# Kernel optimization log

Hardware: AMD Instinct MI355X
Metric: run time of the kernel (lower is better)

Reference implementation:

```python
import jax, jax.numpy as jnp
import numpy as np

EPS_ATTN = 1e-8  # self.eps is undefined in the torch source; standard slot-attention value
LN_EPS = 1e-5


def _ln(x, g=None, b=None, axes=(-1,)):
    m = x.mean(axes, keepdims=True)
    v = ((x - m) ** 2).mean(axes, keepdims=True)
    y = (x - m) * jax.lax.rsqrt(v + LN_EPS)
    return y * g + b if g is not None else y


def setup_inputs() -> dict:
    key = jax.random.key(0)
    ks = jax.random.split(key, 16)
    B, N, S, d, dh = 16, 4096, 8, 64, 128

    def w(k, shape, fan_in):
        return jax.random.normal(k, shape, jnp.float32) / np.float32(np.sqrt(fan_in))

    return {
        "inputs": jax.random.normal(ks[0], (B, N, d + 2), jnp.float32),
        "slots": jax.random.normal(ks[1], (S, d + 4), jnp.float32),
        "Wq": w(ks[2], (d, d), d),
        "Wk": w(ks[3], (d, d), d),
        "Wv": w(ks[4], (d, d), d),
        "Wg": w(ks[5], (d, 2), 2),
        "bg": jnp.zeros((d,), jnp.float32),
        "ln_pos_g": jnp.ones((d,), jnp.float32),
        "ln_pos_b": jnp.zeros((d,), jnp.float32),
        "W1": w(ks[6], (dh, d), d),
        "b1": jnp.zeros((dh,), jnp.float32),
        "W2": w(ks[7], (d, dh), dh),
        "b2": jnp.zeros((d,), jnp.float32),
        "W_ih": w(ks[8], (3 * d, d), d),
        "W_hh": w(ks[9], (3 * d, d), d),
        "b_ih": jnp.zeros((3 * d,), jnp.float32),
        "b_hh": jnp.zeros((3 * d,), jnp.float32),
        "ln_mlp_g": jnp.ones((d,), jnp.float32),
        "ln_mlp_b": jnp.zeros((d,), jnp.float32),
        "W3": w(ks[10], (dh, d), d),
        "b3": jnp.zeros((dh,), jnp.float32),
        "W4": w(ks[11], (d, dh), dh),
        "b4": jnp.zeros((d,), jnp.float32),
        "ln_slot_g": jnp.ones((d,), jnp.float32),
        "ln_slot_b": jnp.zeros((d,), jnp.float32),
        "n_iters": 3,
    }


def reference(inputs, slots, Wq, Wk, Wv, Wg, bg, ln_pos_g, ln_pos_b, W1, b1, W2, b2,
              W_ih, W_hh, b_ih, b_hh, ln_mlp_g, ln_mlp_b, W3, b3, W4, b4,
              ln_slot_g, ln_slot_b, n_iters):
    feats, grids = inputs[..., :-2], inputs[..., -2:]          # (B,N,d), (B,N,2)
    sl, pos, sc = slots[..., :-4], slots[..., -4:-2], slots[..., -2:]
    B, N, _ = feats.shape
    S, d = sl.shape
    scale = d ** (-0.5)

    slots = jnp.broadcast_to(sl, (B, S, d))
    positions = jnp.clip(jnp.broadcast_to(pos, (B, S, 2)), -1.0, 1.0)
    scales = jnp.clip(jnp.broadcast_to(sc, (B, S, 2)), 1e-3, 2.0)

    k = feats @ Wk.T                                           # (B,N,d)
    v = feats @ Wv.T

    def pos_mlp(x):  # LayerNorm -> Linear -> ReLU -> Linear
        h = _ln(x, ln_pos_g, ln_pos_b)
        h = jax.nn.relu(h @ W1.T + b1)
        return h @ W2.T + b2

    for i_iter in range(n_iters + 1):
        rel = (grids[:, :, None] - positions[:, None]) / scales[:, None]  # (B,N,S,2)
        rgp = rel @ Wg.T + bg                                             # (B,N,S,d)
        k_pos = pos_mlp(k[:, :, None] + rgp)                              # (B,N,S,d)
        v_pos = pos_mlp(v[:, :, None] + rgp)

        slots_n = _ln(slots, ln_slot_g, ln_slot_b)
        q = _ln(slots_n, axes=(-2, -1)) @ Wq.T                            # (B,S,d)

        dots = jnp.einsum('bsd,bnsd->bns', q, k_pos) * scale              # (B,N,S)
        attn = jax.nn.softmax(dots, axis=1) + EPS_ATTN
        attn = attn / attn.sum(axis=-1, keepdims=True)

        updates = jnp.einsum('bns,bnsd->bsd', attn, v_pos)                # (B,S,d)
        positions = jnp.einsum('bns,bnp->bsp', attn, grids)               # (B,S,2)
        spread = (grids[:, :, None] - positions[:, None]) ** 2            # (B,N,S,2)
        scales = jnp.clip(jnp.sqrt(jnp.einsum('bns,bnsp->bsp', attn, spread)), 1e-3, 2.0)

        if i_iter < n_iters:
            x = updates.reshape(-1, d)
            h = slots.reshape(-1, d)
            gi = x @ W_ih.T + b_ih
            gh = h @ W_hh.T + b_hh
            i_r, i_z, i_n = jnp.split(gi, 3, axis=-1)
            h_r, h_z, h_n = jnp.split(gh, 3, axis=-1)
            r = jax.nn.sigmoid(i_r + h_r)
            z = jax.nn.sigmoid(i_z + h_z)
            n_g = jnp.tanh(i_n + r * h_n)
            slots = ((1.0 - z) * n_g + z * h).reshape(B, S, d)
            # slot_mlp (no residual in the source)
            hmlp = jax.nn.relu(_ln(slots, ln_mlp_g, ln_mlp_b) @ W3.T + b3)
            slots = hmlp @ W4.T + b4

    return jnp.concatenate([slots, positions, scales], axis=-1)           # (B,S,d+4)
```

## Files before the change

### kernel.cpp

```cpp
#include <hip/hip_runtime.h>
#include <math.h>

#define BB 16
#define NN 4096
#define SS 8
#define DD 64
#define DHH 128
#define CIN 66
#define NITERS 3
#define LN_EPS_F 1e-5f
#define EPS_ATTN_F 1e-8f
#define QSCALE 0.125f
#define LO_SCALE 2048.0f
#define LO_INV 4.8828125e-4f

typedef __attribute__((ext_vector_type(8))) _Float16 half8;
typedef __attribute__((ext_vector_type(4))) float f32x4;
union H8 { half8 v; _Float16 u[8]; };

__device__ __forceinline__ float dot4(float4 a, float4 b) {
    return fmaf(a.x, b.x, fmaf(a.y, b.y, fmaf(a.z, b.z, a.w * b.w)));
}

__device__ __forceinline__ void split_fp16(float z, _Float16& h, _Float16& l) {
    _Float16 hh = (_Float16)z;
    float rem = (z - (float)hh) * LO_SCALE;
    h = hh;
    l = (_Float16)rem;
}

__global__ __launch_bounds__(256) void k_init_slots(
    const float* __restrict__ slots_in, float* __restrict__ slots,
    float* __restrict__ positions, float* __restrict__ scales) {
    int tid = blockIdx.x * 256 + threadIdx.x;
    if (tid < BB * SS * DD) {
        int s = (tid / DD) % SS;
        int c = tid % DD;
        slots[tid] = slots_in[s * 68 + c];
    }
    if (tid < BB * SS * 2) {
        int s = (tid >> 1) & 7;
        int p = tid & 1;
        float po = slots_in[s * 68 + 64 + p];
        positions[tid] = fminf(fmaxf(po, -1.f), 1.f);
        float sc = slots_in[s * 68 + 66 + p];
        scales[tid] = fminf(fmaxf(sc, 1e-3f), 2.f);
    }
}

__global__ __launch_bounds__(256) void k_prep_w(
    const float* __restrict__ W1, const float* __restrict__ lpg,
    const float* __restrict__ lpb, const float* __restrict__ b1,
    const float* __restrict__ Wg,
    float* __restrict__ W1p, float* __restrict__ avec, float* __restrict__ bvec,
    float* __restrict__ s1vec, float* __restrict__ b1p, float* __restrict__ wgc) {
    __shared__ float w1s[128 * 68];
    int tid = threadIdx.x;
    for (int q = 0; q < 8; q++) {
        int flat = q * 1024 + tid * 4;
        int o = flat >> 6, c = flat & 63;
        *(float4*)(w1s + o * 68 + c) = *(const float4*)(W1 + flat);
    }
    __syncthreads();
    if (tid < 128) {
        int o = tid;
        float a = 0.f, bv = 0.f, s1 = 0.f, b1a = b1[o];
        for (int c = 0; c < 64; c++) {
            float w0 = w1s[o * 68 + c];
            float w = w0 * lpg[c];
            W1p[o * 64 + c] = w;
            a = fmaf(w, Wg[2 * c], a);
            bv = fmaf(w, Wg[2 * c + 1], bv);
            s1 += w;
            b1a = fmaf(w0, lpb[c], b1a);
        }
        avec[o] = a; bvec[o] = bv; s1vec[o] = s1; b1p[o] = b1a;
    }
    if (tid == 128) {
        float mwA = 0.f, mwB = 0.f, AA = 0.f, BBv = 0.f, AB = 0.f;
        for (int c = 0; c < 64; c++) {
            float wa = Wg[2 * c], wb = Wg[2 * c + 1];
            mwA += wa; mwB += wb;
            AA = fmaf(wa, wa, AA); BBv = fmaf(wb, wb, BBv); AB = fmaf(wa, wb, AB);
        }
        wgc[0] = mwA * (1.f / 64.f);
        wgc[1] = mwB * (1.f / 64.f);
        wgc[2] = AA * (1.f / 64.f);
        wgc[3] = BBv * (1.f / 64.f);
        wgc[4] = AB * (2.f / 64.f);
    }
}

__global__ __launch_bounds__(256) void k_prep_w2(
    const float* __restrict__ W1p, const float* __restrict__ Wk,
    const float* __restrict__ Wv, const float* __restrict__ bg,
    float* __restrict__ Wall, float* __restrict__ cu) {
    int flat = blockIdx.x * 256 + threadIdx.x;
    int mat = flat >> 13, rem = flat & 8191;
    int o = rem >> 6, c = rem & 63;
    const float* Wm = mat ? Wv : Wk;
    float acc = 0.f;
    for (int d = 0; d < 64; d++)
        acc = fmaf(W1p[o * 64 + d], Wm[d * 64 + c], acc);
    Wall[flat] = acc;
    if (flat < 128) {
        float a = 0.f;
        for (int d = 0; d < 64; d++) a = fmaf(W1p[flat * 64 + d], bg[d], a);
        cu[flat] = a;
    }
}

__global__ __launch_bounds__(256) void k_prep_frag(
    const float* __restrict__ Wall, const float* __restrict__ Wk,
    const float* __restrict__ Wv,
    _Float16* __restrict__ cwh, _Float16* __restrict__ cwl,
    _Float16* __restrict__ mwh, _Float16* __restrict__ mwl) {
    int idx = blockIdx.x * 256 + threadIdx.x;
    if (idx < 2048) {
        int f = idx >> 6, lane = idx & 63;
        int m = f >> 4, rest = f & 15;
        int ot = rest >> 1, ks = rest & 1;
        int o = ot * 16 + (lane & 15);
        int k0 = ks * 32 + (lane >> 4) * 8;
        const float* src = Wall + m * 8192 + o * 64 + k0;
        #pragma unroll
        for (int j = 0; j < 8; j++) {
            _Float16 h, l;
            split_fp16(src[j], h, l);
            cwh[(size_t)f * 512 + lane * 8 + j] = h;
            cwl[(size_t)f * 512 + lane * 8 + j] = l;
        }
    } else if (idx < 3072) {
        int id2 = idx - 2048;
        int f = id2 >> 6, lane = id2 & 63;
        int m = f >> 3, rest = f & 7;
        int ot = rest >> 1, ks = rest & 1;
        int o = ot * 16 + (lane & 15);
        int k0 = ks * 32 + (lane >> 4) * 8;
        const float* src = (m ? Wv : Wk) + o * 64 + k0;
        #pragma unroll
        for (int j = 0; j < 8; j++) {
            _Float16 h, l;
            split_fp16(src[j], h, l);
            mwh[(size_t)f * 512 + lane * 8 + j] = h;
            mwl[(size_t)f * 512 + lane * 8 + j] = l;
        }
    }
}

__global__ __launch_bounds__(256) void k_prep_mfma(
    const float* __restrict__ inp,
    const _Float16* __restrict__ cwh, const _Float16* __restrict__ cwl,
    const _Float16* __restrict__ mwh, const _Float16* __restrict__ mwl,
    const float* __restrict__ cu, const float* __restrict__ bg,
    const float* __restrict__ Wg,
    float* __restrict__ uk, float* __restrict__ uv,
    float* __restrict__ kaux, float* __restrict__ vaux, float* __restrict__ gbuf) {
    __shared__ float T[4][16 * 132];
    int tid = threadIdx.x;
    int wv = tid >> 6, lane = tid & 63;
    int quad = lane >> 4, col = lane & 15;
    int mat = blockIdx.y;
    int rowTile = blockIdx.x * 64 + wv * 16;
    half8 ah[2], al[2];
    {
        int rA = rowTile + col;
        const float* rp = inp + (size_t)rA * CIN + quad * 8;
        #pragma unroll
        for (int ks = 0; ks < 2; ks++) {
            H8 h, l;
            #pragma unroll
            for (int q = 0; q < 4; q++) {
                float2 v = *(const float2*)(rp + ks * 32 + 2 * q);
                split_fp16(v.x, h.u[2 * q], l.u[2 * q]);
                split_fp16(v.y, h.u[2 * q + 1], l.u[2 * q + 1]);
            }
            ah[ks] = h.v; al[ks] = l.v;
        }
    }
    const _Float16* cwhm = cwh + (size_t)mat * 16 * 512;
    const _Float16* cwlm = cwl + (size_t)mat * 16 * 512;
    #pragma unroll
    for (int ot = 0; ot < 8; ot++) {
        f32x4 acc1 = {0.f, 0.f, 0.f, 0.f}, acc2 = {0.f, 0.f, 0.f, 0.f};
        #pragma unroll
        for (int ks = 0; ks < 2; ks++) {
            half8 bh = *(const half8*)(cwhm + (size_t)(ot * 2 + ks) * 512 + lane * 8);
            half8 bl = *(const half8*)(cwlm + (size_t)(ot * 2 + ks) * 512 + lane * 8);
            acc1 = __builtin_amdgcn_mfma_f32_16x16x32_f16(ah[ks], bh, acc1, 0, 0, 0);
            acc2 = __builtin_amdgcn_mfma_f32_16x16x32_f16(al[ks], bh, acc2, 0, 0, 0);
            acc2 = __builtin_amdgcn_mfma_f32_16x16x32_f16(ah[ks], bl, acc2, 0, 0, 0);
        }
        float cuv = cu[ot * 16 + col];
        #pragma unroll
        for (int r = 0; r < 4; r++) {
            float u = fmaf(acc2[r], LO_INV, acc1[r]) + cuv;
            T[wv][(quad * 4 + r) * 132 + ot * 16 + col] = u;
        }
    }
    const _Float16* mwhm = mwh + (size_t)mat * 8 * 512;
    const _Float16* mwlm = mwl + (size_t)mat * 8 * 512;
    float mk[4] = {0.f, 0.f, 0.f, 0.f}, kk2[4] = {0.f, 0.f, 0.f, 0.f};
    float kA[4] = {0.f, 0.f, 0.f, 0.f}, kB[4] = {0.f, 0.f, 0.f, 0.f};
    #pragma unroll
    for (int ot = 0; ot < 4; ot++) {
        f32x4 acc1 = {0.f, 0.f, 0.f, 0.f}, acc2 = {0.f, 0.f, 0.f, 0.f};
        #pragma unroll
        for (int ks = 0; ks < 2; ks++) {
            half8 bh = *(const half8*)(mwhm + (size_t)(ot * 2 + ks) * 512 + lane * 8);
            half8 bl = *(const half8*)(mwlm + (size_t)(ot * 2 + ks) * 512 + lane * 8);
            acc1 = __builtin_amdgcn_mfma_f32_16x16x32_f16(ah[ks], bh, acc1, 0, 0, 0);
            acc2 = __builtin_amdgcn_mfma_f32_16x16x32_f16(al[ks], bh, acc2, 0, 0, 0);
            acc2 = __builtin_amdgcn_mfma_f32_16x16x32_f16(ah[ks], bl, acc2, 0, 0, 0);
        }
        int o = ot * 16 + col;
        float bgo = bg[o], wa = Wg[2 * o], wb = Wg[2 * o + 1];
        #pragma unroll
        for (int r = 0; r < 4; r++) {
            float x = fmaf(acc2[r], LO_INV, acc1[r]) + bgo;
            mk[r] += x; kk2[r] = fmaf(x, x, kk2[r]);
            kA[r] = fmaf(x, wa, kA[r]); kB[r] = fmaf(x, wb, kB[r]);
        }
    }
    #pragma unroll
    for (int off = 1; off <= 8; off <<= 1) {
        #pragma unroll
        for (int r = 0; r < 4; r++) {
            mk[r] += __shfl_xor(mk[r], off, 64);
            kk2[r] += __shfl_xor(kk2[r], off, 64);
            kA[r] += __shfl_xor(kA[r], off, 64);
            kB[r] += __shfl_xor(kB[r], off, 64);
        }
    }
    float* aux = mat ? vaux : kaux;
    if (col == 0) {
        #pragma unroll
        for (int r = 0; r < 4; r++) {
            int row = rowTile + quad * 4 + r;
            float2 g = *(const float2*)(inp + (size_t)row * CIN + 64);
            float4 m1 = {mk[r] * (1.f / 64.f), kk2[r] * (1.f / 64.f),
                         kA[r] * (1.f / 32.f), kB[r] * (1.f / 32.f)};
            float4 m2 = {g.x, g.y, 0.f, 0.f};
            *(float4*)(aux + (size_t)row * 8) = m1;
            *(float4*)(aux + (size_t)row * 8 + 4) = m2;
            if (mat == 0) {
                float2 gw = {g.x, g.y};
                *(float2*)(gbuf + (size_t)row * 2) = gw;
            }
        }
    }
    __syncthreads();
    {
        float* dst = mat ? uv : uk;
        int r = lane >> 2, cseg = (lane & 3) * 32;
        const float* Tr = &T[wv][r * 132 + cseg];
        float* gp = dst + (size_t)(rowTile + r) * 128 + cseg;
        #pragma unroll
        for (int q = 0; q < 8; q++)
            *(float4*)(gp + 4 * q) = *(const float4*)(Tr + 4 * q);
    }
}

__global__ __launch_bounds__(512) void k_slot_prep(
    const float* __restrict__ slots, const float* __restrict__ lsg,
    const float* __restrict__ lsb, const float* __restrict__ Wq,
    const float* __restrict__ W2, const float* __restrict__ b2,
    float* __restrict__ w2q, float* __restrict__ qb2) {
    __shared__ float sn[512];
    __shared__ float qv[SS][64];
    __shared__ float wsum[8], wsum2[8];
    int b = blockIdx.x, t = threadIdx.x;
    int s = t >> 6, c = t & 63;
    float x = slots[(b * SS + s) * DD + c];
    float sum = x;
    for (int off = 32; off; off >>= 1) sum += __shfl_xor(sum, off, 64);
    float m = sum * (1.f / 64.f);
    float dv = x - m;
    float vs = dv * dv;
    for (int off = 32; off; off >>= 1) vs += __shfl_xor(vs, off, 64);
    float y = dv * rsqrtf(vs * (1.f / 64.f) + LN_EPS_F) * lsg[c] + lsb[c];
    float s1 = y, s2 = y * y;
    for (int off = 32; off; off >>= 1) { s1 += __shfl_xor(s1, off, 64); s2 += __shfl_xor(s2, off, 64); }
    if (c == 0) { wsum[s] = s1; wsum2[s] = s2; }
    __syncthreads();
    float ts1 = 0.f, ts2 = 0.f;
    #pragma unroll
    for (int i = 0; i < 8; i++) { ts1 += wsum[i]; ts2 += wsum2[i]; }
    float gm = ts1 * (1.f / 512.f);
    float gv = ts2 * (1.f / 512.f) - gm * gm;
    sn[t] = (y - gm) * rsqrtf(gv + LN_EPS_F);
    __syncthreads();
    float acc = 0.f;
    for (int j4 = 0; j4 < 64; j4 += 4)
        acc += dot4(*(const float4*)&sn[s * 64 + j4], *(const float4*)(Wq + c * 64 + j4));
    qv[s][c] = acc;
    __syncthreads();
    float a0 = 0.f, a1 = 0.f;
    for (int cc = 0; cc < 64; cc++) {
        float qc = qv[s][cc];
        a0 = fmaf(qc, W2[cc * DHH + c], a0);
        a1 = fmaf(qc, W2[cc * DHH + c + 64], a1);
    }
    w2q[(b * SS + s) * DHH + c] = a0 * QSCALE;
    w2q[(b * SS + s) * DHH + c + 64] = a1 * QSCALE;
    float qb = qv[s][c] * b2[c];
    for (int off = 32; off; off >>= 1) qb += __shfl_xor(qb, off, 64);
    if (c == 0) qb2[b * SS + s] = qb * QSCALE;
}

__global__ __launch_bounds__(256) void k_pass1(
    const float* __restrict__ uk, const float* __restrict__ kaux,
    const float* __restrict__ positions, const float* __restrict__ scales,
    const float* __restrict__ avec, const float* __restrict__ bvec,
    const float* __restrict__ s1vec, const float* __restrict__ b1p,
    const float* __restrict__ wgc, const float* __restrict__ w2q,
    const float* __restrict__ qb2, float* __restrict__ dots) {
    int tid = threadIdx.x;
    int chunk = blockIdx.x, b = blockIdx.y;
    int wv = tid >> 6, lane = tid & 63, rh = lane >> 5, ol = lane & 31;
    int o4 = ol * 4;
    float4 a4 = *(const float4*)(avec + o4);
    float4 bv4 = *(const float4*)(bvec + o4);
    float4 s14 = *(const float4*)(s1vec + o4);
    float4 b14 = *(const float4*)(b1p + o4);
    float mwA = wgc[0], mwB = wgc[1], AA = wgc[2], BBc = wgc[3], AB2 = wgc[4];
    float p0[8], p1[8], rc0[8], rc1[8], qb[8];
    float4 wq[8];
    #pragma unroll
    for (int s = 0; s < 8; s++) {
        int bs = b * 8 + s;
        p0[s] = positions[bs * 2]; p1[s] = positions[bs * 2 + 1];
        rc0[s] = 1.f / scales[bs * 2]; rc1[s] = 1.f / scales[bs * 2 + 1];
        qb[s] = qb2[bs];
        wq[s] = *(const float4*)(w2q + (size_t)bs * DHH + o4);
    }
    int row0 = chunk * 64 + wv * 16 + rh;
    size_t rg = (size_t)b * NN + row0;
    float4 m1 = *(const float4*)(kaux + rg * 8);
    float4 m2 = *(const float4*)(kaux + rg * 8 + 4);
    float4 u4 = *(const float4*)(uk + rg * 128 + o4);
    for (int st = 0; st < 8; st++) {
        float4 n1, n2, nu;
        if (st < 7) {
            size_t rgn = rg + (size_t)(st + 1) * 2;
            n1 = *(const float4*)(kaux + rgn * 8);
            n2 = *(const float4*)(kaux + rgn * 8 + 4);
            nu = *(const float4*)(uk + rgn * 128 + o4);
        }
        int row = row0 + st * 2;
        #pragma unroll
        for (int s = 0; s < 8; s++) {
            float rel0 = (m2.x - p0[s]) * rc0[s];
            float rel1 = (m2.y - p1[s]) * rc1[s];
            float m = fmaf(rel1, mwB, fmaf(rel0, mwA, m1.x));
            float q2 = fmaf(rel0, fmaf(rel0, AA, m1.z), m1.y);
            q2 = fmaf(rel1, fmaf(rel1, BBc, m1.w), q2);
            q2 = fmaf(rel0 * rel1, AB2, q2);
            float var = fmaf(-m, m, q2);
            float rstd = rsqrtf(fmaxf(var, 0.f) + LN_EPS_F);
            float p = 0.f, t, h;
            t = fmaf(-m, s14.x, u4.x); t = fmaf(rel0, a4.x, t); t = fmaf(rel1, bv4.x, t);
            h = fmaf(rstd, t, b14.x); p = fmaf(fmaxf(h, 0.f), wq[s].x, p);
            t = fmaf(-m, s14.y, u4.y); t = fmaf(rel0, a4.y, t); t = fmaf(rel1, bv4.y, t);
            h = fmaf(rstd, t, b14.y); p = fmaf(fmaxf(h, 0.f), wq[s].y, p);
            t = fmaf(-m, s14.z, u4.z); t = fmaf(rel0, a4.z, t); t = fmaf(rel1, bv4.z, t);
            h = fmaf(rstd, t, b14.z); p = fmaf(fmaxf(h, 0.f), wq[s].z, p);
            t = fmaf(-m, s14.w, u4.w); t = fmaf(rel0, a4.w, t); t = fmaf(rel1, bv4.w, t);
            h = fmaf(rstd, t, b14.w); p = fmaf(fmaxf(h, 0.f), wq[s].w, p);
            p += __shfl_xor(p, 1, 64);
            p += __shfl_xor(p, 2, 64);
            p += __shfl_xor(p, 4, 64);
            p += __shfl_xor(p, 8, 64);
            p += __shfl_xor(p, 16, 64);
            if (ol == 0)
                dots[(size_t)(b * 8 + s) * NN + row] = p + qb[s];
        }
        m1 = n1; m2 = n2; u4 = nu;
    }
}

__global__ __launch_bounds__(256) void k_pass2(
    const float* __restrict__ uv, const float* __restrict__ vaux,
    const float* __restrict__ positions, const float* __restrict__ scales,
    const float* __restrict__ avec, const float* __restrict__ bvec,
    const float* __restrict__ s1vec, const float* __restrict__ b1p,
    const float* __restrict__ wgc, const float* __restrict__ attn,
    float* __restrict__ H) {
    __shared__ float Hw[4 * 1024];
    int tid = threadIdx.x;
    int chunk = blockIdx.x, b = blockIdx.y;
    int wv = tid >> 6, lane = tid & 63, rh = lane >> 5, ol = lane & 31;
    int o4 = ol * 4;
    float4 a4 = *(const float4*)(avec + o4);
    float4 bv4 = *(const float4*)(bvec + o4);
    float4 s14 = *(const float4*)(s1vec + o4);
    float4 b14 = *(const float4*)(b1p + o4);
    float mwA = wgc[0], mwB = wgc[1], AA = wgc[2], BBc = wgc[3], AB2 = wgc[4];
    float p0[8], p1[8], rc0[8], rc1[8];
    #pragma unroll
    for (int s = 0; s < 8; s++) {
        int bs = b * 8 + s;
        p0[s] = positions[bs * 2]; p1[s] = positions[bs * 2 + 1];
        rc0[s] = 1.f / scales[bs * 2]; rc1[s] = 1.f / scales[bs * 2 + 1];
    }
    float hq[8][4];
    #pragma unroll
    for (int s = 0; s < 8; s++)
        #pragma unroll
        for (int c = 0; c < 4; c++) hq[s][c] = 0.f;
    int row0 = chunk * 64 + wv * 16 + rh;
    size_t rg = (size_t)b * NN + row0;
    float4 m1 = *(const float4*)(vaux + rg * 8);
    float4 m2 = *(const float4*)(vaux + rg * 8 + 4);
    float4 u4 = *(const float4*)(uv + rg * 128 + o4);
    for (int st = 0; st < 8; st++) {
        float4 n1, n2, nu;
        if (st < 7) {
            size_t rgn = rg + (size_t)(st + 1) * 2;
            n1 = *(const float4*)(vaux + rgn * 8);
            n2 = *(const float4*)(vaux + rgn * 8 + 4);
            nu = *(const float4*)(uv + rgn * 128 + o4);
        }
        int row = row0 + st * 2;
        #pragma unroll
        for (int s = 0; s < 8; s++) {
            float ar = attn[(size_t)(b * 8 + s) * NN + row];
            float rel0 = (m2.x - p0[s]) * rc0[s];
            float rel1 = (m2.y - p1[s]) * rc1[s];
            float m = fmaf(rel1, mwB, fmaf(rel0, mwA, m1.x));
            float q2 = fmaf(rel0, fmaf(rel0, AA, m1.z), m1.y);
            q2 = fmaf(rel1, fmaf(rel1, BBc, m1.w), q2);
            q2 = fmaf(rel0 * rel1, AB2, q2);
            float var = fmaf(-m, m, q2);
            float rstd = rsqrtf(fmaxf(var, 0.f) + LN_EPS_F);
            float t, h;
            t = fmaf(-m, s14.x, u4.x); t = fmaf(rel0, a4.x, t); t = fmaf(rel1, bv4.x, t);
            h = fmaf(rstd, t, b14.x); hq[s][0] = fmaf(ar, fmaxf(h, 0.f), hq[s][0]);
            t = fmaf(-m, s14.y, u4.y); t = fmaf(rel0, a4.y, t); t = fmaf(rel1, bv4.y, t);
            h = fmaf(rstd, t, b14.y); hq[s][1] = fmaf(ar, fmaxf(h, 0.f), hq[s][1]);
            t = fmaf(-m, s14.z, u4.z); t = fmaf(rel0, a4.z, t); t = fmaf(rel1, bv4.z, t);
            h = fmaf(rstd, t, b14.z); hq[s][2] = fmaf(ar, fmaxf(h, 0.f), hq[s][2]);
            t = fmaf(-m, s14.w, u4.w); t = fmaf(rel0, a4.w, t); t = fmaf(rel1, bv4.w, t);
            h = fmaf(rstd, t, b14.w); hq[s][3] = fmaf(ar, fmaxf(h, 0.f), hq[s][3]);
        }
        m1 = n1; m2 = n2; u4 = nu;
    }
    #pragma unroll
    for (int s = 0; s < 8; s++)
        #pragma unroll
        for (int c = 0; c < 4; c++)
            hq[s][c] += __shfl_xor(hq[s][c], 32, 64);
    if (lane < 32) {
        #pragma unroll
        for (int s = 0; s < 8; s++) {
            float4 st = {hq[s][0], hq[s][1], hq[s][2], hq[s][3]};
            *(float4*)(Hw + wv * 1024 + s * 128 + o4) = st;
        }
    }
    __syncthreads();
    #pragma unroll
    for (int q = 0; q < 4; q++) {
        int flat = q * 256 + tid;
        float sum = Hw[flat] + Hw[1024 + flat] + Hw[2048 + flat] + Hw[3072 + flat];
        atomicAdd(&H[(size_t)b * 8 * DHH + flat], sum);
    }
}

__global__ __launch_bounds__(256) void k_softmax_ms(
    const float* __restrict__ dots, float* __restrict__ Mv, float* __restrict__ Lv,
    float* __restrict__ H) {
    __shared__ float red[4];
    int bs = blockIdx.x, t = threadIdx.x;
    if (t < 128) H[(size_t)bs * DHH + t] = 0.f;
    const float* dp = dots + (size_t)bs * NN;
    float mx = -1e30f;
    #pragma unroll
    for (int it = 0; it < 4; it++) {
        float4 d = *(const float4*)(dp + it * 1024 + t * 4);
        mx = fmaxf(mx, fmaxf(fmaxf(d.x, d.y), fmaxf(d.z, d.w)));
    }
    for (int off = 32; off; off >>= 1) mx = fmaxf(mx, __shfl_xor(mx, off, 64));
    if ((t & 63) == 0) red[t >> 6] = mx;
    __syncthreads();
    float M = fmaxf(fmaxf(red[0], red[1]), fmaxf(red[2], red[3]));
    __syncthreads();
    float sm = 0.f;
    #pragma unroll
    for (int it = 0; it < 4; it++) {
        float4 d = *(const float4*)(dp + it * 1024 + t * 4);
        sm += expf(d.x - M) + expf(d.y - M) + expf(d.z - M) + expf(d.w - M);
    }
    for (int off = 32; off; off >>= 1) sm += __shfl_xor(sm, off, 64);
    if ((t & 63) == 0) red[t >> 6] = sm;
    __syncthreads();
    if (t == 0) { Mv[bs] = M; Lv[bs] = red[0] + red[1] + red[2] + red[3]; }
}

__global__ __launch_bounds__(256) void k_attn(
    const float* __restrict__ dots, const float* __restrict__ Mv,
    const float* __restrict__ Lv, float* __restrict__ attn) {
    int chunk = blockIdx.x, b = blockIdx.y;
    int n = chunk * 256 + threadIdx.x;
    float a[8];
    float rs = 0.f;
    #pragma unroll
    for (int s = 0; s < 8; s++) {
        int bs = b * 8 + s;
        float d = dots[(size_t)bs * NN + n];
        a[s] = expf(d - Mv[bs]) * (1.f / Lv[bs]) + EPS_ATTN_F;
        rs += a[s];
    }
    float inv = 1.f / rs;
    #pragma unroll
    for (int s = 0; s < 8; s++)
        attn[(size_t)(b * 8 + s) * NN + n] = a[s] * inv;
}

__global__ __launch_bounds__(256) void k_stats(
    const float* __restrict__ attn, const float* __restrict__ gbuf,
    float* __restrict__ positions, float* __restrict__ scales,
    float* __restrict__ stats) {
    __shared__ float red[4][5];
    int bs = blockIdx.x, b = bs >> 3, t = threadIdx.x;
    const float* ap = attn + (size_t)bs * NN;
    const float* gb = gbuf + (size_t)b * NN * 2;
    float v0 = 0.f, v1 = 0.f, v2 = 0.f, v3 = 0.f, v4 = 0.f;
    #pragma unroll
    for (int it = 0; it < 4; it++) {
        int n0 = it * 1024 + t * 4;
        float4 av = *(const float4*)(ap + n0);
        float4 g1 = *(const float4*)(gb + (size_t)n0 * 2);
        float4 g2 = *(const float4*)(gb + (size_t)n0 * 2 + 4);
        v0 += av.x + av.y + av.z + av.w;
        v1 = fmaf(av.x, g1.x, fmaf(av.y, g1.z, fmaf(av.z, g2.x, fmaf(av.w, g2.z, v1))));
        v2 = fmaf(av.x, g1.y, fmaf(av.y, g1.w, fmaf(av.z, g2.y, fmaf(av.w, g2.w, v2))));
        v3 = fmaf(av.x, g1.x * g1.x, fmaf(av.y, g1.z * g1.z, fmaf(av.z, g2.x * g2.x, fmaf(av.w, g2.z * g2.z, v3))));
        v4 = fmaf(av.x, g1.y * g1.y, fmaf(av.y, g1.w * g1.w, fmaf(av.z, g2.y * g2.y, fmaf(av.w, g2.w * g2.w, v4))));
    }
    for (int off = 32; off; off >>= 1) {
        v0 += __shfl_xor(v0, off, 64); v1 += __shfl_xor(v1, off, 64);
        v2 += __shfl_xor(v2, off, 64); v3 += __shfl_xor(v3, off, 64);
        v4 += __shfl_xor(v4, off, 64);
    }
    if ((t & 63) == 0) {
        int w = t >> 6;
        red[w][0] = v0; red[w][1] = v1; red[w][2] = v2; red[w][3] = v3; red[w][4] = v4;
    }
    __syncthreads();
    if (t == 0) {
        float A0 = red[0][0] + red[1][0] + red[2][0] + red[3][0];
        float A1x = red[0][1] + red[1][1] + red[2][1] + red[3][1];
        float A1y = red[0][2] + red[1][2] + red[2][2] + red[3][2];
        float A2x = red[0][3] + red[1][3] + red[2][3] + red[3][3];
        float A2y = red[0][4] + red[1][4] + red[2][4] + red[3][4];
        positions[bs * 2 + 0] = A1x;
        positions[bs * 2 + 1] = A1y;
        float sx = A2x - A1x * A1x * (2.f - A0);
        float sy = A2y - A1y * A1y * (2.f - A0);
        scales[bs * 2 + 0] = fminf(fmaxf(sqrtf(fmaxf(sx, 0.f)), 1e-3f), 2.f);
        scales[bs * 2 + 1] = fminf(fmaxf(sqrtf(fmaxf(sy, 0.f)), 1e-3f), 2.f);
        stats[bs] = A0;
    }
}

__global__ __launch_bounds__(64) void k_gru_mlp(
    const float* __restrict__ H, const float* __restrict__ stats,
    const float* __restrict__ W2, const float* __restrict__ b2,
    const float* __restrict__ W_ih, const float* __restrict__ W_hh,
    const float* __restrict__ b_ih, const float* __restrict__ b_hh,
    const float* __restrict__ lmg, const float* __restrict__ lmb,
    const float* __restrict__ W3, const float* __restrict__ b3,
    const float* __restrict__ W4, const float* __restrict__ b4,
    float* __restrict__ slots) {
    int bs = blockIdx.x;
    int c = threadIdx.x;
    __shared__ float hl[DHH], ul[DD], sl[DD], yl[DD], hml[DHH];
    hl[c] = H[bs * DHH + c];
    hl[c + 64] = H[bs * DHH + 64 + c];
    float hold = slots[bs * DD + c];
    sl[c] = hold;
    __syncthreads();
    float A0 = stats[bs];
    float u = A0 * b2[c];
    for (int o = 0; o < DHH; o += 4) {
        float4 w = *(const float4*)(W2 + c * DHH + o);
        u = fmaf(w.x, hl[o], fmaf(w.y, hl[o + 1], fmaf(w.z, hl[o + 2], fmaf(w.w, hl[o + 3], u))));
    }
    ul[c] = u;
    __syncthreads();
    float gir = b_ih[c], giz = b_ih[64 + c], gin = b_ih[128 + c];
    float ghr = b_hh[c], ghz = b_hh[64 + c], ghn = b_hh[128 + c];
    for (int k4 = 0; k4 < DD; k4 += 4) {
        float4 uu = *(const float4*)(ul + k4);
        float4 hh = *(const float4*)(sl + k4);
        gir += dot4(uu, *(const float4*)(W_ih + c * DD + k4));
        giz += dot4(uu, *(const float4*)(W_ih + (64 + c) * DD + k4));
        gin += dot4(uu, *(const float4*)(W_ih + (128 + c) * DD + k4));
        ghr += dot4(hh, *(const float4*)(W_hh + c * DD + k4));
        ghz += dot4(hh, *(const float4*)(W_hh + (64 + c) * DD + k4));
        ghn += dot4(hh, *(const float4*)(W_hh + (128 + c) * DD + k4));
    }
    float rg = 1.f / (1.f + expf(-(gir + ghr)));
    float zg = 1.f / (1.f + expf(-(giz + ghz)));
    float ng = tanhf(gin + rg * ghn);
    float snew = (1.f - zg) * ng + zg * hold;
    float sum = snew;
    for (int off = 32; off; off >>= 1) sum += __shfl_xor(sum, off, 64);
    float m = sum * (1.f / 64.f);
    float dv = snew - m;
    float vv = dv * dv;
    for (int off = 32; off; off >>= 1) vv += __shfl_xor(vv, off, 64);
    yl[c] = dv * rsqrtf(vv * (1.f / 64.f) + LN_EPS_F) * lmg[c] + lmb[c];
    __syncthreads();
    float h0 = b3[c], h1 = b3[64 + c];
    for (int k4 = 0; k4 < DD; k4 += 4) {
        float4 yy = *(const float4*)(yl + k4);
        h0 += dot4(yy, *(const float4*)(W3 + c * DD + k4));
        h1 += dot4(yy, *(const float4*)(W3 + (64 + c) * DD + k4));
    }
    hml[c] = fmaxf(h0, 0.f);
    hml[64 + c] = fmaxf(h1, 0.f);
    __syncthreads();
    float outv = b4[c];
    for (int o4 = 0; o4 < DHH; o4 += 4) {
        float4 hm4 = *(const float4*)(hml + o4);
        outv += dot4(hm4, *(const float4*)(W4 + c * DHH + o4));
    }
    slots[bs * DD + c] = outv;
}

__global__ __launch_bounds__(256) void k_write_out(
    const float* __restrict__ slots, const float* __restrict__ positions,
    const float* __restrict__ scales, float* __restrict__ out) {
    int tid = blockIdx.x * 256 + threadIdx.x;
    if (tid >= BB * SS * 68) return;
    int bs = tid / 68, c = tid % 68;
    float v;
    if (c < 64) v = slots[bs * 64 + c];
    else if (c < 66) v = positions[bs * 2 + (c - 64)];
    else v = scales[bs * 2 + (c - 66)];
    out[tid] = v;
}

extern "C" void kernel_launch(void* const* d_in, const int* in_sizes, int n_in,
                              void* d_out, int out_size, void* d_ws, size_t ws_size,
                              hipStream_t stream) {
    (void)in_sizes; (void)n_in; (void)out_size; (void)ws_size;
    const float* inp = (const float*)d_in[0];
    const float* slots_in = (const float*)d_in[1];
    const float* Wq = (const float*)d_in[2];
    const float* Wk = (const float*)d_in[3];
    const float* Wv = (const float*)d_in[4];
    const float* Wg = (const float*)d_in[5];
    const float* bg = (const float*)d_in[6];
    const float* lpg = (const float*)d_in[7];
    const float* lpb = (const float*)d_in[8];
    const float* W1 = (const float*)d_in[9];
    const float* b1 = (const float*)d_in[10];
    const float* W2 = (const float*)d_in[11];
    const float* b2 = (const float*)d_in[12];
    const float* W_ih = (const float*)d_in[13];
    const float* W_hh = (const float*)d_in[14];
    const float* b_ih = (const float*)d_in[15];
    const float* b_hh = (const float*)d_in[16];
    const float* lmg = (const float*)d_in[17];
    const float* lmb = (const float*)d_in[18];
    const float* W3 = (const float*)d_in[19];
    const float* b3 = (const float*)d_in[20];
    const float* W4 = (const float*)d_in[21];
    const float* b4 = (const float*)d_in[22];
    const float* lsg = (const float*)d_in[23];
    const float* lsb = (const float*)d_in[24];
    float* out = (float*)d_out;
    float* ws = (float*)d_ws;

    const size_t NR = (size_t)BB * NN;
    size_t o_uk = 0;
    size_t o_uv = o_uk + NR * 128;
    size_t o_kaux = o_uv + NR * 128;
    size_t o_vaux = o_kaux + NR * 8;
    size_t o_gbuf = o_vaux + NR * 8;
    size_t o_dots = o_gbuf + NR * 2;
    size_t o_attn = o_dots + NR * SS;
    size_t o_slots = o_attn + NR * SS;
    size_t o_pos = o_slots + BB * SS * DD;
    size_t o_scl = o_pos + BB * SS * 2;
    size_t o_w2q = o_scl + BB * SS * 2;
    size_t o_qb2 = o_w2q + BB * SS * DHH;
    size_t o_Mv = o_qb2 + BB * SS;
    size_t o_Lv = o_Mv + BB * SS;
    size_t o_H = o_Lv + BB * SS;
    size_t o_stats = o_H + BB * SS * DHH;
    size_t o_W1p = o_stats + BB * SS;
    size_t o_avec = o_W1p + DHH * DD;
    size_t o_bvec = o_avec + DHH;
    size_t o_s1v = o_bvec + DHH;
    size_t o_b1p = o_s1v + DHH;
    size_t o_wgc = o_b1p + DHH;
    size_t o_Wall = o_wgc + 8;
    size_t o_cu = o_Wall + 2 * DHH * DD;
    size_t o_cwh = o_cu + DHH;
    size_t o_cwl = o_cwh + 8192;
    size_t o_mwh = o_cwl + 8192;
    size_t o_mwl = o_mwh + 4096;

    float* uk = ws + o_uk;
    float* uv = ws + o_uv;
    float* kaux = ws + o_kaux;
    float* vaux = ws + o_vaux;
    float* gbuf = ws + o_gbuf;
    float* dots = ws + o_dots;
    float* attn = ws + o_attn;
    float* slots = ws + o_slots;
    float* positions = ws + o_pos;
    float* scales = ws + o_scl;
    float* w2q = ws + o_w2q;
    float* qb2 = ws + o_qb2;
    float* Mv = ws + o_Mv;
    float* Lv = ws + o_Lv;
    float* H = ws + o_H;
    float* stats = ws + o_stats;
    float* W1p = ws + o_W1p;
    float* avec = ws + o_avec;
    float* bvec = ws + o_bvec;
    float* s1v = ws + o_s1v;
    float* b1p = ws + o_b1p;
    float* wgc = ws + o_wgc;
    float* Wall = ws + o_Wall;
    float* cu = ws + o_cu;
    _Float16* cwh = (_Float16*)(ws + o_cwh);
    _Float16* cwl = (_Float16*)(ws + o_cwl);
    _Float16* mwh = (_Float16*)(ws + o_mwh);
    _Float16* mwl = (_Float16*)(ws + o_mwl);

    k_init_slots<<<32, 256, 0, stream>>>(slots_in, slots, positions, scales);
    k_prep_w<<<1, 256, 0, stream>>>(W1, lpg, lpb, b1, Wg, W1p, avec, bvec, s1v, b1p, wgc);
    k_prep_w2<<<64, 256, 0, stream>>>(W1p, Wk, Wv, bg, Wall, cu);
    k_prep_frag<<<12, 256, 0, stream>>>(Wall, Wk, Wv, cwh, cwl, mwh, mwl);
    k_prep_mfma<<<dim3(1024, 2), 256, 0, stream>>>(inp, cwh, cwl, mwh, mwl,
                                                   cu, bg, Wg, uk, uv, kaux, vaux, gbuf);

    for (int it = 0; it <= NITERS; ++it) {
        k_slot_prep<<<BB, 512, 0, stream>>>(slots, lsg, lsb, Wq, W2, b2, w2q, qb2);
        k_pass1<<<dim3(64, BB), 256, 0, stream>>>(uk, kaux, positions, scales,
                                                  avec, bvec, s1v, b1p, wgc, w2q, qb2, dots);
        k_softmax_ms<<<BB * SS, 256, 0, stream>>>(dots, Mv, Lv, H);
        k_attn<<<dim3(16, BB), 256, 0, stream>>>(dots, Mv, Lv, attn);
        if (it < NITERS) {
            k_pass2<<<dim3(64, BB), 256, 0, stream>>>(uv, vaux, positions, scales,
                                                      avec, bvec, s1v, b1p, wgc, attn, H);
            k_stats<<<BB * SS, 256, 0, stream>>>(attn, gbuf, positions, scales, stats);
            k_gru_mlp<<<BB * SS, 64, 0, stream>>>(H, stats, W2, b2, W_ih, W_hh, b_ih, b_hh,
                                                  lmg, lmb, W3, b3, W4, b4, slots);
        } else {
            k_stats<<<BB * SS, 256, 0, stream>>>(attn, gbuf, positions, scales, stats);
        }
    }
    k_write_out<<<34, 256, 0, stream>>>(slots, positions, scales, out);
}
```

Baseline: 458.0 us.

## Fuse attention normalization with position/scale stats and write MFMA outputs directly

Merges the attention normalization and per-slot statistics kernels so that weighted sums of the grid coordinates are reduced while attn is produced, then accumulated with atomics into a small buffer. Positions and scales are derived later in the GRU kernel and the output kernel, which removes one pass over attn and one launch per iteration. The MFMA prep kernel now stores results straight to global memory instead of staging them through shared memory. The softmax uses the fast __expf intrinsic. The changes add atomic ordering nondeterminism, slight exp precision loss, and possibly less coalesced stores in the prep kernel.

```diff
diff --git a/kernel.cpp b/kernel.cpp
--- a/kernel.cpp
+++ b/kernel.cpp
@@ -156,7 +156,6 @@
     const float* __restrict__ Wg,
     float* __restrict__ uk, float* __restrict__ uv,
     float* __restrict__ kaux, float* __restrict__ vaux, float* __restrict__ gbuf) {
-    __shared__ float T[4][16 * 132];
     int tid = threadIdx.x;
     int wv = tid >> 6, lane = tid & 63;
     int quad = lane >> 4, col = lane & 15;
@@ -180,6 +179,8 @@
     }
     const _Float16* cwhm = cwh + (size_t)mat * 16 * 512;
     const _Float16* cwlm = cwl + (size_t)mat * 16 * 512;
+    float* dst = mat ? uv : uk;
+    float* outb = dst + (size_t)(rowTile + quad * 4) * 128 + col;
     #pragma unroll
     for (int ot = 0; ot < 8; ot++) {
         f32x4 acc1 = {0.f, 0.f, 0.f, 0.f}, acc2 = {0.f, 0.f, 0.f, 0.f};
@@ -193,10 +194,8 @@
         }
         float cuv = cu[ot * 16 + col];
         #pragma unroll
-        for (int r = 0; r < 4; r++) {
-            float u = fmaf(acc2[r], LO_INV, acc1[r]) + cuv;
-            T[wv][(quad * 4 + r) * 132 + ot * 16 + col] = u;
-        }
+        for (int r = 0; r < 4; r++)
+            outb[(size_t)r * 128 + ot * 16] = fmaf(acc2[r], LO_INV, acc1[r]) + cuv;
     }
     const _Float16* mwhm = mwh + (size_t)mat * 8 * 512;
     const _Float16* mwlm = mwl + (size_t)mat * 8 * 512;
@@ -248,16 +247,6 @@
                 *(float2*)(gbuf + (size_t)row * 2) = gw;
             }
         }
-    }
-    __syncthreads();
-    {
-        float* dst = mat ? uv : uk;
-        int r = lane >> 2, cseg = (lane & 3) * 32;
-        const float* Tr = &T[wv][r * 132 + cseg];
-        float* gp = dst + (size_t)(rowTile + r) * 128 + cseg;
-        #pragma unroll
-        for (int q = 0; q < 8; q++)
-            *(float4*)(gp + 4 * q) = *(const float4*)(Tr + 4 * q);
     }
 }
 
@@ -468,10 +457,11 @@
 
 __global__ __launch_bounds__(256) void k_softmax_ms(
     const float* __restrict__ dots, float* __restrict__ Mv, float* __restrict__ Lv,
-    float* __restrict__ H) {
+    float* __restrict__ H, float* __restrict__ sacc) {
     __shared__ float red[4];
     int bs = blockIdx.x, t = threadIdx.x;
     if (t < 128) H[(size_t)bs * DHH + t] = 0.f;
+    if (t < 8) sacc[bs * 8 + t] = 0.f;
     const float* dp = dots + (size_t)bs * NN;
     float mx = -1e30f;
     #pragma unroll
@@ -488,7 +478,7 @@
     #pragma unroll
     for (int it = 0; it < 4; it++) {
         float4 d = *(const float4*)(dp + it * 1024 + t * 4);
-        sm += expf(d.x - M) + expf(d.y - M) + expf(d.z - M) + expf(d.w - M);
+        sm += __expf(d.x - M) + __expf(d.y - M) + __expf(d.z - M) + __expf(d.w - M);
     }
     for (int off = 32; off; off >>= 1) sm += __shfl_xor(sm, off, 64);
     if ((t & 63) == 0) red[t >> 6] = sm;
@@ -496,91 +486,84 @@
     if (t == 0) { Mv[bs] = M; Lv[bs] = red[0] + red[1] + red[2] + red[3]; }
 }
 
-__global__ __launch_bounds__(256) void k_attn(
+__global__ __launch_bounds__(256) void k_attn_stats(
     const float* __restrict__ dots, const float* __restrict__ Mv,
-    const float* __restrict__ Lv, float* __restrict__ attn) {
+    const float* __restrict__ Lv, const float* __restrict__ gbuf,
+    float* __restrict__ attn, float* __restrict__ sacc) {
+    __shared__ float red[4][40];
     int chunk = blockIdx.x, b = blockIdx.y;
-    int n = chunk * 256 + threadIdx.x;
+    int t = threadIdx.x;
+    int n = chunk * 256 + t;
+    float2 g = *(const float2*)(gbuf + (size_t)(b * NN + n) * 2);
+    float gx2 = g.x * g.x, gy2 = g.y * g.y;
     float a[8];
     float rs = 0.f;
     #pragma unroll
     for (int s = 0; s < 8; s++) {
         int bs = b * 8 + s;
         float d = dots[(size_t)bs * NN + n];
-        a[s] = expf(d - Mv[bs]) * (1.f / Lv[bs]) + EPS_ATTN_F;
+        a[s] = __expf(d - Mv[bs]) * (1.f / Lv[bs]) + EPS_ATTN_F;
         rs += a[s];
     }
     float inv = 1.f / rs;
-    #pragma unroll
-    for (int s = 0; s < 8; s++)
-        attn[(size_t)(b * 8 + s) * NN + n] = a[s] * inv;
-}
-
-__global__ __launch_bounds__(256) void k_stats(
-    const float* __restrict__ attn, const float* __restrict__ gbuf,
-    float* __restrict__ positions, float* __restrict__ scales,
-    float* __restrict__ stats) {
-    __shared__ float red[4][5];
-    int bs = blockIdx.x, b = bs >> 3, t = threadIdx.x;
-    const float* ap = attn + (size_t)bs * NN;
-    const float* gb = gbuf + (size_t)b * NN * 2;
-    float v0 = 0.f, v1 = 0.f, v2 = 0.f, v3 = 0.f, v4 = 0.f;
-    #pragma unroll
-    for (int it = 0; it < 4; it++) {
-        int n0 = it * 1024 + t * 4;
-        float4 av = *(const float4*)(ap + n0);
-        float4 g1 = *(const float4*)(gb + (size_t)n0 * 2);
-        float4 g2 = *(const float4*)(gb + (size_t)n0 * 2 + 4);
-        v0 += av.x + av.y + av.z + av.w;
-        v1 = fmaf(av.x, g1.x, fmaf(av.y, g1.z, fmaf(av.z, g2.x, fmaf(av.w, g2.z, v1))));
-        v2 = fmaf(av.x, g1.y, fmaf(av.y, g1.w, fmaf(av.z, g2.y, fmaf(av.w, g2.w, v2))));
-        v3 = fmaf(av.x, g1.x * g1.x, fmaf(av.y, g1.z * g1.z, fmaf(av.z, g2.x * g2.x, fmaf(av.w, g2.z * g2.z, v3))));
-        v4 = fmaf(av.x, g1.y * g1.y, fmaf(av.y, g1.w * g1.w, fmaf(av.z, g2.y * g2.y, fmaf(av.w, g2.w * g2.w, v4))));
-    }
-    for (int off = 32; off; off >>= 1) {
-        v0 += __shfl_xor(v0, off, 64); v1 += __shfl_xor(v1, off, 64);
-        v2 += __shfl_xor(v2, off, 64); v3 += __shfl_xor(v3, off, 64);
-        v4 += __shfl_xor(v4, off, 64);
-    }
-    if ((t & 63) == 0) {
-        int w = t >> 6;
-        red[w][0] = v0; red[w][1] = v1; red[w][2] = v2; red[w][3] = v3; red[w][4] = v4;
-    }
-    __syncthreads();
-    if (t == 0) {
-        float A0 = red[0][0] + red[1][0] + red[2][0] + red[3][0];
-        float A1x = red[0][1] + red[1][1] + red[2][1] + red[3][1];
-        float A1y = red[0][2] + red[1][2] + red[2][2] + red[3][2];
-        float A2x = red[0][3] + red[1][3] + red[2][3] + red[3][3];
-        float A2y = red[0][4] + red[1][4] + red[2][4] + red[3][4];
-        positions[bs * 2 + 0] = A1x;
-        positions[bs * 2 + 1] = A1y;
-        float sx = A2x - A1x * A1x * (2.f - A0);
-        float sy = A2y - A1y * A1y * (2.f - A0);
-        scales[bs * 2 + 0] = fminf(fmaxf(sqrtf(fmaxf(sx, 0.f)), 1e-3f), 2.f);
-        scales[bs * 2 + 1] = fminf(fmaxf(sqrtf(fmaxf(sy, 0.f)), 1e-3f), 2.f);
-        stats[bs] = A0;
+    float v[8][5];
+    #pragma unroll
+    for (int s = 0; s < 8; s++) {
+        float av = a[s] * inv;
+        attn[(size_t)(b * 8 + s) * NN + n] = av;
+        v[s][0] = av;
+        v[s][1] = av * g.x;  v[s][2] = av * g.y;
+        v[s][3] = av * gx2;  v[s][4] = av * gy2;
+    }
+    #pragma unroll
+    for (int off = 1; off <= 32; off <<= 1)
+        #pragma unroll
+        for (int s = 0; s < 8; s++)
+            #pragma unroll
+            for (int j = 0; j < 5; j++)
+                v[s][j] += __shfl_xor(v[s][j], off, 64);
+    int lane = t & 63, wv = t >> 6;
+    if (lane == 0) {
+        #pragma unroll
+        for (int s = 0; s < 8; s++)
+            #pragma unroll
+            for (int j = 0; j < 5; j++)
+                red[wv][s * 5 + j] = v[s][j];
+    }
+    __syncthreads();
+    if (t < 40) {
+        float sum = red[0][t] + red[1][t] + red[2][t] + red[3][t];
+        int s = t / 5, j = t % 5;
+        atomicAdd(&sacc[(b * 8 + s) * 8 + j], sum);
     }
 }
 
 __global__ __launch_bounds__(64) void k_gru_mlp(
-    const float* __restrict__ H, const float* __restrict__ stats,
+    const float* __restrict__ H, const float* __restrict__ sacc,
     const float* __restrict__ W2, const float* __restrict__ b2,
     const float* __restrict__ W_ih, const float* __restrict__ W_hh,
     const float* __restrict__ b_ih, const float* __restrict__ b_hh,
     const float* __restrict__ lmg, const float* __restrict__ lmb,
     const float* __restrict__ W3, const float* __restrict__ b3,
     const float* __restrict__ W4, const float* __restrict__ b4,
-    float* __restrict__ slots) {
+    float* __restrict__ slots, float* __restrict__ positions,
+    float* __restrict__ scales) {
     int bs = blockIdx.x;
     int c = threadIdx.x;
     __shared__ float hl[DHH], ul[DD], sl[DD], yl[DD], hml[DHH];
+    float A0 = sacc[bs * 8 + 0];
+    if (c < 2) {
+        float A1 = sacc[bs * 8 + 1 + c];
+        float A2 = sacc[bs * 8 + 3 + c];
+        positions[bs * 2 + c] = A1;
+        float sx = A2 - A1 * A1 * (2.f - A0);
+        scales[bs * 2 + c] = fminf(fmaxf(sqrtf(fmaxf(sx, 0.f)), 1e-3f), 2.f);
+    }
     hl[c] = H[bs * DHH + c];
     hl[c + 64] = H[bs * DHH + 64 + c];
     float hold = slots[bs * DD + c];
     sl[c] = hold;
     __syncthreads();
-    float A0 = stats[bs];
     float u = A0 * b2[c];
     for (int o = 0; o < DHH; o += 4) {
         float4 w = *(const float4*)(W2 + c * DHH + o);
@@ -630,15 +613,24 @@
 }
 
 __global__ __launch_bounds__(256) void k_write_out(
-    const float* __restrict__ slots, const float* __restrict__ positions,
-    const float* __restrict__ scales, float* __restrict__ out) {
+    const float* __restrict__ slots, const float* __restrict__ sacc,
+    float* __restrict__ out) {
     int tid = blockIdx.x * 256 + threadIdx.x;
     if (tid >= BB * SS * 68) return;
     int bs = tid / 68, c = tid % 68;
     float v;
-    if (c < 64) v = slots[bs * 64 + c];
-    else if (c < 66) v = positions[bs * 2 + (c - 64)];
-    else v = scales[bs * 2 + (c - 66)];
+    if (c < 64) {
+        v = slots[bs * 64 + c];
+    } else if (c < 66) {
+        v = sacc[bs * 8 + 1 + (c - 64)];
+    } else {
+        int p = c - 66;
+        float A0 = sacc[bs * 8 + 0];
+        float A1 = sacc[bs * 8 + 1 + p];
+        float A2 = sacc[bs * 8 + 3 + p];
+        float sx = A2 - A1 * A1 * (2.f - A0);
+        v = fminf(fmaxf(sqrtf(fmaxf(sx, 0.f)), 1e-3f), 2.f);
+    }
     out[tid] = v;
 }
 
@@ -690,8 +682,8 @@
     size_t o_Mv = o_qb2 + BB * SS;
     size_t o_Lv = o_Mv + BB * SS;
     size_t o_H = o_Lv + BB * SS;
-    size_t o_stats = o_H + BB * SS * DHH;
-    size_t o_W1p = o_stats + BB * SS;
+    size_t o_sacc = o_H + BB * SS * DHH;
+    size_t o_W1p = o_sacc + BB * SS * 8;
     size_t o_avec = o_W1p + DHH * DD;
     size_t o_bvec = o_avec + DHH;
     size_t o_s1v = o_bvec + DHH;
@@ -719,7 +711,7 @@
     float* Mv = ws + o_Mv;
     float* Lv = ws + o_Lv;
     float* H = ws + o_H;
-    float* stats = ws + o_stats;
+    float* sacc = ws + o_sacc;
     float* W1p = ws + o_W1p;
     float* avec = ws + o_avec;
     float* bvec = ws + o_bvec;
@@ -744,17 +736,15 @@
         k_slot_prep<<<BB, 512, 0, stream>>>(slots, lsg, lsb, Wq, W2, b2, w2q, qb2);
         k_pass1<<<dim3(64, BB), 256, 0, stream>>>(uk, kaux, positions, scales,
                                                   avec, bvec, s1v, b1p, wgc, w2q, qb2, dots);
-        k_softmax_ms<<<BB * SS, 256, 0, stream>>>(dots, Mv, Lv, H);
-        k_attn<<<dim3(16, BB), 256, 0, stream>>>(dots, Mv, Lv, attn);
+        k_softmax_ms<<<BB * SS, 256, 0, stream>>>(dots, Mv, Lv, H, sacc);
+        k_attn_stats<<<dim3(16, BB), 256, 0, stream>>>(dots, Mv, Lv, gbuf, attn, sacc);
         if (it < NITERS) {
             k_pass2<<<dim3(64, BB), 256, 0, stream>>>(uv, vaux, positions, scales,
                                                       avec, bvec, s1v, b1p, wgc, attn, H);
-            k_stats<<<BB * SS, 256, 0, stream>>>(attn, gbuf, positions, scales, stats);
-            k_gru_mlp<<<BB * SS, 64, 0, stream>>>(H, stats, W2, b2, W_ih, W_hh, b_ih, b_hh,
-                                                  lmg, lmb, W3, b3, W4, b4, slots);
-        } else {
-            k_stats<<<BB * SS, 256, 0, stream>>>(attn, gbuf, positions, scales, stats);
-        }
-    }
-    k_write_out<<<34, 256, 0, stream>>>(slots, positions, scales, out);
-}
+            k_gru_mlp<<<BB * SS, 64, 0, stream>>>(H, sacc, W2, b2, W_ih, W_hh, b_ih, b_hh,
+                                                  lmg, lmb, W3, b3, W4, b4,
+                                                  slots, positions, scales);
+        }
+    }
+    k_write_out<<<34, 256, 0, stream>>>(slots, sacc, out);
+}
```

Result: faster. 443.3 us (-3.2%).
